# Performance work log

Measured on AMD Instinct MI355X. Metric: run time of the kernel, lower is better.

The kernel has to match this reference:

```python
import jax, jax.numpy as jnp
import numpy as np

B, S, D = 4, 1024, 2048
NH, HD = 16, 128  # nhead, head_dim
SCALE = HD ** -0.5


def setup_inputs() -> dict:
    key = jax.random.key(0)
    ks = jax.random.split(key, 7)
    query = jax.random.normal(ks[0], (B, S, D), dtype=jnp.float32)
    key_t = jax.random.normal(ks[1], (B, S, D), dtype=jnp.float32)
    value = jax.random.normal(ks[2], (B, S, D), dtype=jnp.float32)
    # qkv_proj: Linear(D, 3D) with bias; out_proj: Linear(D, D) with bias
    Wqkv = jax.random.normal(ks[3], (3 * D, D), dtype=jnp.float32) * (D ** -0.5)
    bqkv = jnp.zeros((3 * D,), dtype=jnp.float32)
    Wout = jax.random.normal(ks[4], (D, D), dtype=jnp.float32) * (D ** -0.5)
    bout = jnp.zeros((D,), dtype=jnp.float32)
    return {"query": query, "key": key_t, "value": value,
            "Wqkv": Wqkv, "bqkv": bqkv, "Wout": Wout, "bout": bout}


def reference(query, key, value, Wqkv, bqkv, Wout, bout):
    # NOTE: module ignores `key`/`value` args; qkv comes from query alone.
    b, s, d = query.shape
    qkv = query @ Wqkv.T + bqkv                       # (B,S,3D)
    q, k, v = jnp.split(qkv, 3, axis=-1)
    q = q.reshape(b, s, NH, HD).transpose(0, 2, 1, 3) * SCALE  # (B,H,S,hd)
    k = k.reshape(b, s, NH, HD).transpose(0, 2, 1, 3)          # (B,H,S,hd)
    # faithful replication of the module's odd v permutation:
    v = v.reshape(b, s, HD, NH).transpose(0, 2, 1, 3)          # (B,hd,S,H)
    v = v.reshape(b, s, NH * HD).reshape(b, s, NH, HD).transpose(0, 2, 1, 3)  # (B,H,S,hd)
    scores = jnp.einsum('bhqd,bhkd->bhqk', q, k)               # (B,H,S,S)
    causal = jnp.triu(jnp.ones((s, s), dtype=bool), k=1)
    scores = jnp.where(causal, -jnp.inf, scores)
    attn = jax.nn.softmax(scores.astype(jnp.float32), axis=-1).astype(query.dtype)
    out = jnp.einsum('bhqk,bhkd->bhqd', attn, v)               # (B,H,S,hd)
    out = out.transpose(0, 2, 1, 3).reshape(b, s, d)
    return out @ Wout.T + bout
```

## Files before the change

kernel.cpp:

```cpp
#include <hip/hip_runtime.h>
#include <hip/hip_bf16.h>
#include <stdint.h>

typedef __bf16 bf16x8 __attribute__((ext_vector_type(8)));
typedef float  floatx4 __attribute__((ext_vector_type(4)));

#define NEG_BIG (-1e30f)

#define GLD16(g, l) __builtin_amdgcn_global_load_lds(                         \
    (__attribute__((address_space(1))) void*)(g),                             \
    (__attribute__((address_space(3))) void*)(l), 16, 0, 0)

__device__ __forceinline__ void cvt16(const float* __restrict__ s,
                                      __hip_bfloat16* __restrict__ d) {
    float4 f[4];
#pragma unroll
    for (int i = 0; i < 4; i++) f[i] = ((const float4*)s)[i];
    union { __hip_bfloat16 h[16]; uint4 u[2]; } o;
#pragma unroll
    for (int i = 0; i < 4; i++) {
        o.h[4 * i + 0] = __float2bfloat16(f[i].x);
        o.h[4 * i + 1] = __float2bfloat16(f[i].y);
        o.h[4 * i + 2] = __float2bfloat16(f[i].z);
        o.h[4 * i + 3] = __float2bfloat16(f[i].w);
    }
    ((uint4*)d)[0] = o.u[0];
    ((uint4*)d)[1] = o.u[1];
}

__global__ __launch_bounds__(256)
void cvt3_f32_bf16(const float* __restrict__ a, size_t na8,
                   const float* __restrict__ b, size_t nb8,
                   const float* __restrict__ c, size_t nc8,
                   __hip_bfloat16* __restrict__ da,
                   __hip_bfloat16* __restrict__ db,
                   __hip_bfloat16* __restrict__ dc)
{
    const size_t total  = na8 + nb8 + nc8;
    const size_t stride = (size_t)gridDim.x * blockDim.x;
    for (size_t idx = (size_t)blockIdx.x * blockDim.x + threadIdx.x;
         idx < total; idx += stride) {
        const float* s; __hip_bfloat16* d; size_t o;
        if (idx < na8)            { s = a; d = da; o = idx; }
        else if (idx < na8 + nb8) { s = b; d = db; o = idx - na8; }
        else                      { s = c; d = dc; o = idx - na8 - nb8; }
        const float4 f0 = ((const float4*)s)[o * 2 + 0];
        const float4 f1 = ((const float4*)s)[o * 2 + 1];
        union { __hip_bfloat16 h[8]; uint4 u; } z;
        z.h[0] = __float2bfloat16(f0.x); z.h[1] = __float2bfloat16(f0.y);
        z.h[2] = __float2bfloat16(f0.z); z.h[3] = __float2bfloat16(f0.w);
        z.h[4] = __float2bfloat16(f1.x); z.h[5] = __float2bfloat16(f1.y);
        z.h[6] = __float2bfloat16(f1.z); z.h[7] = __float2bfloat16(f1.w);
        ((uint4*)d)[o] = z.u;
    }
}

template <bool OUT_F32>
__global__ __launch_bounds__(512, 2)
void gemm8p_nt_bias(const __hip_bfloat16* __restrict__ A,
                    const __hip_bfloat16* __restrict__ B,
                    const float* __restrict__ bias, void* __restrict__ Cv,
                    int M, int N, int K, int lda, int ldb, int nby)
{
    __shared__ __align__(16) __hip_bfloat16 Asm[2][128 * 64];
    __shared__ __align__(16) __hip_bfloat16 Bsm[2][256 * 64];

    const int nwg = gridDim.x, cpx = nwg >> 3;
    const int flat = blockIdx.x;
    const int swz  = (flat & 7) * cpx + (flat >> 3);
    const int by = swz % nby, bx = swz / nby;
    const int m0 = by * 128, n0 = bx * 256;

    const int t    = threadIdx.x;
    const int wave = t >> 6, lane = t & 63;
    const int quad = lane >> 4, l16 = lane & 15;
    const int wr   = wave >> 2, wc = wave & 3;
    const int NT   = K >> 6;

    const int l8 = lane >> 3;
    const int g_ = (lane & 7) ^ l8;
    const int aRowBase = (wave >> 2) * 64 + (wave & 3) * 8;
    const int bRowBase = wave * 8;

    auto stageA = [&](int tk, int j, int buf) {
        GLD16(A + (size_t)(m0 + aRowBase + j * 32 + l8) * lda + tk * 64 + g_ * 8,
              &Asm[buf][0] + (aRowBase + j * 32) * 64);
    };
    auto stageB = [&](int tk, int j, int buf) {
        GLD16(B + (size_t)(n0 + bRowBase + j * 64 + l8) * ldb + tk * 64 + g_ * 8,
              &Bsm[buf][0] + (bRowBase + j * 64) * 64);
    };

    const int g0 = (quad ^ (l16 & 7)) << 3;

    floatx4 acc[4][4];
    const floatx4 zero = {0.f, 0.f, 0.f, 0.f};
#pragma unroll
    for (int mi = 0; mi < 4; mi++)
#pragma unroll
        for (int ni = 0; ni < 4; ni++) acc[mi][ni] = zero;

    stageA(0, 0, 0); stageA(0, 1, 0);
    stageB(0, 0, 0); stageB(0, 1, 0); stageB(0, 2, 0); stageB(0, 3, 0);
    if (NT > 1) {
        stageA(1, 0, 1); stageB(1, 0, 1); stageB(1, 1, 1);
        asm volatile("s_waitcnt vmcnt(3)" ::: "memory");
    } else {
        asm volatile("s_waitcnt vmcnt(0)" ::: "memory");
    }
    __syncthreads();

    int cb = 0;
    for (int tk = 0; tk < NT; ++tk, cb ^= 1) {
        const __hip_bfloat16* Ab = &Asm[cb][0];
        const __hip_bfloat16* Bb = &Bsm[cb][0];
        const int nb = cb ^ 1;

        bf16x8 af[2][2], bfr[4][2];
#pragma unroll
        for (int i = 0; i < 2; i++)
#pragma unroll
            for (int ks = 0; ks < 2; ks++)
                af[i][ks] = *(const bf16x8*)(
                    Ab + (wr * 64 + i * 16 + l16) * 64 + (g0 ^ (ks ? 32 : 0)));
#pragma unroll
        for (int ni = 0; ni < 4; ni++)
#pragma unroll
            for (int ks = 0; ks < 2; ks++)
                bfr[ni][ks] = *(const bf16x8*)(
                    Bb + (wc * 64 + ni * 16 + l16) * 64 + (g0 ^ (ks ? 32 : 0)));
        if (tk + 1 < NT) {
            stageA(tk + 1, 1, nb); stageB(tk + 1, 2, nb); stageB(tk + 1, 3, nb);
        }
        __builtin_amdgcn_s_barrier();
        asm volatile("s_waitcnt lgkmcnt(0)" ::: "memory");
        __builtin_amdgcn_s_setprio(1);
#pragma unroll
        for (int ks = 0; ks < 2; ks++)
#pragma unroll
            for (int i = 0; i < 2; i++)
#pragma unroll
                for (int ni = 0; ni < 4; ni++)
                    acc[i][ni] = __builtin_amdgcn_mfma_f32_16x16x32_bf16(
                        af[i][ks], bfr[ni][ks], acc[i][ni], 0, 0, 0);
        __builtin_amdgcn_s_setprio(0);
        __builtin_amdgcn_s_barrier();

#pragma unroll
        for (int i = 0; i < 2; i++)
#pragma unroll
            for (int ks = 0; ks < 2; ks++)
                af[i][ks] = *(const bf16x8*)(
                    Ab + (wr * 64 + (2 + i) * 16 + l16) * 64 + (g0 ^ (ks ? 32 : 0)));
        if (tk + 2 < NT) {
            stageA(tk + 2, 0, cb); stageB(tk + 2, 0, cb); stageB(tk + 2, 1, cb);
        }
        __builtin_amdgcn_s_barrier();
        asm volatile("s_waitcnt lgkmcnt(0)" ::: "memory");
        __builtin_amdgcn_s_setprio(1);
#pragma unroll
        for (int ks = 0; ks < 2; ks++)
#pragma unroll
            for (int i = 0; i < 2; i++)
#pragma unroll
                for (int ni = 0; ni < 4; ni++)
                    acc[2 + i][ni] = __builtin_amdgcn_mfma_f32_16x16x32_bf16(
                        af[i][ks], bfr[ni][ks], acc[2 + i][ni], 0, 0, 0);
        __builtin_amdgcn_s_setprio(0);
        if (tk + 2 < NT)
            asm volatile("s_waitcnt vmcnt(3)" ::: "memory");
        else if (tk + 1 < NT)
            asm volatile("s_waitcnt vmcnt(0)" ::: "memory");
        __builtin_amdgcn_s_barrier();
    }

#pragma unroll
    for (int mi = 0; mi < 4; mi++) {
        const int row = m0 + wr * 64 + mi * 16 + quad * 4;
#pragma unroll
        for (int ni = 0; ni < 4; ni++) {
            const int col = n0 + wc * 64 + ni * 16 + l16;
            const float bv = bias[col];
#pragma unroll
            for (int r = 0; r < 4; r++) {
                const float v = acc[mi][ni][r] + bv;
                if (OUT_F32)
                    ((float*)Cv)[(size_t)(row + r) * N + col] = v;
                else
                    ((__hip_bfloat16*)Cv)[(size_t)(row + r) * N + col] =
                        __float2bfloat16(v);
            }
        }
    }
}

template <bool A_F32, bool B_F32, bool OUT_F32>
__global__ __launch_bounds__(256, 2)
void gemm_nt_bias(const void* __restrict__ Av, const void* __restrict__ Bv,
                  const float* __restrict__ bias, void* __restrict__ Cv,
                  int M, int N, int K, int lda, int ldb)
{
    __shared__ __align__(16) __hip_bfloat16 Asm[128 * 32];
    __shared__ __align__(16) __hip_bfloat16 Bsm[128 * 32];
    const int m0   = blockIdx.y * 128;
    const int n0   = blockIdx.x * 128;
    const int t    = threadIdx.x;
    const int wave = t >> 6, lane = t & 63;
    const int quad = lane >> 4, l16 = lane & 15;
    const int wr   = wave >> 1, wc = wave & 1;

    floatx4 zero = {0.f, 0.f, 0.f, 0.f};
    floatx4 acc[4][4];
    for (int i = 0; i < 4; i++)
        for (int j = 0; j < 4; j++) acc[i][j] = zero;

    for (int k0 = 0; k0 < K; k0 += 32) {
        if (A_F32) {
            const float* A = (const float*)Av;
            const int row = t >> 1, half = t & 1;
            cvt16(A + (size_t)(m0 + row) * lda + k0 + half * 16,
                  Asm + row * 32 + half * 16);
        } else {
            const __hip_bfloat16* A = (const __hip_bfloat16*)Av;
            for (int j = 0; j < 2; ++j) {
                const int chunk = (wave * 2 + j) * 64 + lane;
                const int row   = chunk >> 2;
                const int kc    = chunk & 3;
                GLD16(A + (size_t)(m0 + row) * lda + k0 + kc * 8,
                      Asm + (wave * 2 + j) * 512);
            }
        }
        if (B_F32) {
            const float* B = (const float*)Bv;
            const int row = t >> 1, half = t & 1;
            cvt16(B + (size_t)(n0 + row) * ldb + k0 + half * 16,
                  Bsm + row * 32 + half * 16);
        } else {
            const __hip_bfloat16* B = (const __hip_bfloat16*)Bv;
            for (int j = 0; j < 2; ++j) {
                const int chunk = (wave * 2 + j) * 64 + lane;
                const int row   = chunk >> 2;
                const int kc    = chunk & 3;
                GLD16(B + (size_t)(n0 + row) * ldb + k0 + kc * 8,
                      Bsm + (wave * 2 + j) * 512);
            }
        }
        __syncthreads();

        bf16x8 af[4], bf[4];
        for (int i = 0; i < 4; i++) {
            af[i] = *(const bf16x8*)(Asm + (wr * 64 + i * 16 + l16) * 32 + quad * 8);
            bf[i] = *(const bf16x8*)(Bsm + (wc * 64 + i * 16 + l16) * 32 + quad * 8);
        }
        for (int mi = 0; mi < 4; mi++)
            for (int ni = 0; ni < 4; ni++)
                acc[mi][ni] = __builtin_amdgcn_mfma_f32_16x16x32_bf16(
                    af[mi], bf[ni], acc[mi][ni], 0, 0, 0);
        __syncthreads();
    }

    for (int mi = 0; mi < 4; mi++) {
        const int row = m0 + wr * 64 + mi * 16 + quad * 4;
        for (int ni = 0; ni < 4; ni++) {
            const int col = n0 + wc * 64 + ni * 16 + l16;
            const float bv = bias[col];
            for (int r = 0; r < 4; r++) {
                const float v = acc[mi][ni][r] + bv;
                if (OUT_F32)
                    ((float*)Cv)[(size_t)(row + r) * N + col] = v;
                else
                    ((__hip_bfloat16*)Cv)[(size_t)(row + r) * N + col] =
                        __float2bfloat16(v);
            }
        }
    }
}

__global__ __launch_bounds__(256)
void permute_v(const __hip_bfloat16* __restrict__ QKV,
               __hip_bfloat16* __restrict__ Vpt)
{
    __shared__ __align__(16) __hip_bfloat16 S[64 * 64];
    const int blk = blockIdx.x;
    const int sb = blk & 31, h = (blk >> 5) & 15, b = blk >> 9;
    const int t = threadIdx.x;

    for (int j = 0; j < 2; j++) {
        const int chunk = j * 256 + t;
        const int lrow  = chunk >> 3;
        const int lcol  = (chunk & 7) * 8;
        const int r8 = lrow >> 3, jj = lrow & 7;
        const int srow = r8 * 128 + h * 8 + jj;
        const int scol = sb * 64 + lcol;
        *(uint4*)(S + chunk * 8) =
            *(const uint4*)(QKV + ((size_t)(b * 1024) + srow) * 6144 + 4096 + scol);
    }
    __syncthreads();

    const size_t obase = (((size_t)(b * 16 + h)) * 32 + sb) * 4096;
    for (int i = 0; i < 16; i++) {
        const int lin = t + 256 * i;
        const int hd = lin >> 5, ss = lin & 31;
        Vpt[obase + lin] =
            S[((ss & 7) * 8 + (hd >> 4)) * 64 + (ss >> 3) * 16 + (hd & 15)];
    }
}

__global__ __launch_bounds__(256, 2)
void flash_attn(const __hip_bfloat16* __restrict__ QKV,
                const __hip_bfloat16* __restrict__ Vpt,
                __hip_bfloat16* __restrict__ O)
{
    __shared__ __align__(16) __hip_bfloat16 Kt[2][64 * 128];
    __shared__ __align__(16) __hip_bfloat16 Vt[2][2 * 128 * 32];
    __shared__ __align__(16) __hip_bfloat16 Pl[64 * 64];

    const int bid  = blockIdx.x;
    const int pair = bid >> 6;
    const int g    = bid & 63;
    const int b    = g >> 4, h = g & 15;
    const int t    = threadIdx.x;
    const int wave = t >> 6, lane = t & 63;
    const int quad = lane >> 4, l16 = lane & 15;
    const float scale = 0.08838834764831845f;

    const int    rowb  = b * 1024;
    const size_t vbase = (((size_t)(b * 16 + h)) * 32) * 4096;
    const floatx4 zero = {0.f, 0.f, 0.f, 0.f};

    auto stageK = [&](int tk, int bufi) {
        const int kv0 = tk * 64;
        __hip_bfloat16* dst = &Kt[bufi][0];
#pragma unroll
        for (int j = 0; j < 4; j++) {
            const int c0 = (wave * 4 + j) * 64 + lane;
            const int r  = c0 >> 4;
            const int gg = (c0 & 15) ^ (r & 7);
            GLD16(QKV + ((size_t)(rowb + kv0 + r)) * 6144 + 2048 + h * 128 + gg * 8,
                  dst + (wave * 4 + j) * 512);
        }
    };
    auto stageV = [&](int tk, int bufi) {
        const __hip_bfloat16* src = Vpt + vbase + (size_t)(tk * 2) * 4096;
        __hip_bfloat16* dst = &Vt[bufi][0];
#pragma unroll
        for (int j = 0; j < 4; j++) {
            const int c0   = (wave * 4 + j) * 64 + lane;
            const int half = c0 >> 9, w = c0 & 511;
            const int r    = w >> 2;
            const int gg   = (w & 3) ^ (r & 3);
            GLD16(src + half * 4096 + r * 32 + gg * 8,
                  dst + (wave * 4 + j) * 512);
        }
    };

    for (int ph = 0; ph < 2; ++ph) {
        const int qb = ph ? (15 - pair) * 64 : pair * 64;
        const int nt = ph ? 16 - pair       : pair + 1;

        bf16x8 qf[4];
        {
            const size_t rb = ((size_t)(rowb + qb + wave * 16 + l16)) * 6144 + h * 128;
#pragma unroll
            for (int kc = 0; kc < 4; kc++)
                qf[kc] = *(const bf16x8*)(QKV + rb + kc * 32 + quad * 8);
        }

        float m_i[4], l_i[4];
        floatx4 oacc[8];
#pragma unroll
        for (int r = 0; r < 4; r++) { m_i[r] = NEG_BIG; l_i[r] = 0.f; }
#pragma unroll
        for (int ni = 0; ni < 8; ni++) oacc[ni] = zero;

        stageK(0, 0); stageV(0, 0);

        for (int tk = 0; tk < nt; ++tk) {
            const int cur = tk & 1;
            if (tk + 1 < nt) {
                stageK(tk + 1, cur ^ 1); stageV(tk + 1, cur ^ 1);
                asm volatile("s_waitcnt vmcnt(8)" ::: "memory");
            } else {
                asm volatile("s_waitcnt vmcnt(0)" ::: "memory");
            }
            __builtin_amdgcn_s_barrier();
            asm volatile("" ::: "memory");

            const __hip_bfloat16* Kb = &Kt[cur][0];
            const __hip_bfloat16* Vb = &Vt[cur][0];
            const int kv0 = tk * 64;

            floatx4 sc[4];
#pragma unroll
            for (int cbk = 0; cbk < 4; cbk++) {
                floatx4 s = zero;
                const int r  = cbk * 16 + l16;
                const int sw = r & 7;
#pragma unroll
                for (int kc = 0; kc < 4; kc++) {
                    bf16x8 kf = *(const bf16x8*)(
                        Kb + r * 128 + (((kc * 4 + quad) ^ sw) << 3));
                    s = __builtin_amdgcn_mfma_f32_16x16x32_bf16(qf[kc], kf, s, 0, 0, 0);
                }
                sc[cbk] = s;
            }

            const int qrow = qb + wave * 16 + quad * 4;
            if (tk == nt - 1) {
#pragma unroll
                for (int rr = 0; rr < 4; rr++)
#pragma unroll
                    for (int cbk = 0; cbk < 4; cbk++) {
                        const int col = kv0 + cbk * 16 + l16;
                        const float v = sc[cbk][rr] * scale;
                        sc[cbk][rr] = (col > qrow + rr) ? NEG_BIG : v;
                    }
            } else {
#pragma unroll
                for (int rr = 0; rr < 4; rr++)
#pragma unroll
                    for (int cbk = 0; cbk < 4; cbk++) sc[cbk][rr] *= scale;
            }
            float mx[4];
#pragma unroll
            for (int rr = 0; rr < 4; rr++)
                mx[rr] = fmaxf(fmaxf(sc[0][rr], sc[1][rr]),
                               fmaxf(sc[2][rr], sc[3][rr]));
#pragma unroll
            for (int off = 1; off < 16; off <<= 1)
#pragma unroll
                for (int rr = 0; rr < 4; rr++)
                    mx[rr] = fmaxf(mx[rr], __shfl_xor(mx[rr], off));

            float alpha[4], rsum[4];
#pragma unroll
            for (int rr = 0; rr < 4; rr++) {
                const float mnew = fmaxf(m_i[rr], mx[rr]);
                alpha[rr] = __expf(m_i[rr] - mnew);
                m_i[rr] = mnew;
                float acc = 0.f;
#pragma unroll
                for (int cbk = 0; cbk < 4; cbk++) {
                    const float pv = __expf(sc[cbk][rr] - mnew);
                    sc[cbk][rr] = pv;
                    acc += pv;
                }
                rsum[rr] = acc;
            }
#pragma unroll
            for (int off = 1; off < 16; off <<= 1)
#pragma unroll
                for (int rr = 0; rr < 4; rr++)
                    rsum[rr] += __shfl_xor(rsum[rr], off);
#pragma unroll
            for (int rr = 0; rr < 4; rr++)
                l_i[rr] = l_i[rr] * alpha[rr] + rsum[rr];
#pragma unroll
            for (int ni = 0; ni < 8; ni++)
#pragma unroll
                for (int rr = 0; rr < 4; rr++) oacc[ni][rr] *= alpha[rr];

#pragma unroll
            for (int cbk = 0; cbk < 4; cbk++)
#pragma unroll
                for (int rr = 0; rr < 4; rr++) {
                    const int row = wave * 16 + quad * 4 + rr;
                    const int col = cbk * 16 + l16;
                    Pl[row * 64 + ((((col >> 3) ^ (row & 7)) << 3) | (col & 7))] =
                        __float2bfloat16(sc[cbk][rr]);
                }
            asm volatile("s_waitcnt lgkmcnt(0)" ::: "memory");

            const int prow = wave * 16 + l16;
            bf16x8 pf[2];
#pragma unroll
            for (int kc = 0; kc < 2; kc++)
                pf[kc] = *(const bf16x8*)(
                    Pl + prow * 64 + (((kc * 4 + quad) ^ (prow & 7)) << 3));
#pragma unroll
            for (int ni = 0; ni < 8; ni++) {
                const int vr = ni * 16 + l16;
#pragma unroll
                for (int kc = 0; kc < 2; kc++) {
                    bf16x8 vf = *(const bf16x8*)(
                        Vb + kc * 4096 + vr * 32 + (((quad ^ (vr & 3))) << 3));
                    oacc[ni] = __builtin_amdgcn_mfma_f32_16x16x32_bf16(
                        pf[kc], vf, oacc[ni], 0, 0, 0);
                }
            }

            asm volatile("" ::: "memory");
            __builtin_amdgcn_s_barrier();
            asm volatile("" ::: "memory");
        }

        float inv[4];
#pragma unroll
        for (int rr = 0; rr < 4; rr++) inv[rr] = 1.0f / l_i[rr];
#pragma unroll
        for (int ni = 0; ni < 8; ni++)
#pragma unroll
            for (int rr = 0; rr < 4; rr++) {
                const int row = qb + wave * 16 + quad * 4 + rr;
                O[((size_t)rowb + row) * 6144 + 4096 + h * 128 + ni * 16 + l16] =
                    __float2bfloat16(oacc[ni][rr] * inv[rr]);
            }
    }
}

extern "C" void kernel_launch(void* const* d_in, const int* in_sizes, int n_in,
                              void* d_out, int out_size, void* d_ws, size_t ws_size,
                              hipStream_t stream) {
    const float* query = (const float*)d_in[0];
    const float* Wqkv = (const float*)d_in[3];
    const float* bqkv = (const float*)d_in[4];
    const float* Wout = (const float*)d_in[5];
    const float* bout = (const float*)d_in[6];
    float* out = (float*)d_out;

    const size_t MB = 1048576;
    char* ws = (char*)d_ws;
    __hip_bfloat16* QKV = (__hip_bfloat16*)ws;
    __hip_bfloat16* Vpt = (__hip_bfloat16*)(ws + 48 * MB);
    __hip_bfloat16* Att = QKV + 4096;

    dim3 blk(256);

    if (ws_size >= 113 * MB) {
        __hip_bfloat16* Qbf     = (__hip_bfloat16*)(ws + 64 * MB);
        __hip_bfloat16* Wqkv_bf = (__hip_bfloat16*)(ws + 80 * MB);
        __hip_bfloat16* Wout_bf = (__hip_bfloat16*)(ws + 104 * MB);

        cvt3_f32_bf16<<<dim3(2048), blk, 0, stream>>>(
            query, (size_t)4096 * 2048 / 8,
            Wqkv,  (size_t)6144 * 2048 / 8,
            Wout,  (size_t)2048 * 2048 / 8,
            Qbf, Wqkv_bf, Wout_bf);
        gemm8p_nt_bias<false><<<dim3(768), dim3(512), 0, stream>>>(
            Qbf, Wqkv_bf, bqkv, QKV, 4096, 6144, 2048, 2048, 2048, 32);
        permute_v<<<dim3(2048), blk, 0, stream>>>(QKV, Vpt);
        flash_attn<<<dim3(512), blk, 0, stream>>>(QKV, Vpt, QKV);
        gemm8p_nt_bias<true><<<dim3(256), dim3(512), 0, stream>>>(
            Att, Wout_bf, bout, out, 4096, 2048, 2048, 6144, 2048, 32);
    } else {
        gemm_nt_bias<true, true, false><<<dim3(48, 32), blk, 0, stream>>>(
            query, Wqkv, bqkv, QKV, 4096, 6144, 2048, 2048, 2048);
        permute_v<<<dim3(2048), blk, 0, stream>>>(QKV, Vpt);
        flash_attn<<<dim3(512), blk, 0, stream>>>(QKV, Vpt, QKV);
        gemm_nt_bias<false, true, true><<<dim3(16, 32), blk, 0, stream>>>(
            Att, Wout, bout, out, 4096, 2048, 2048, 6144, 2048);
    }
}
```

Baseline: 381.1 us.

## Add 128x192-tile 256-thread GEMM for QKV projection with split-phase pipelining

Introduces a new bf16 NT GEMM kernel using 128x192 output tiles, 4 waves of 256 threads, and a two-phase per-k-tile schedule that interleaves global-to-LDS staging of the next tiles with MFMA work on half the A rows. The QKV projection launch switches from the 512-thread 128x256 kernel (768 blocks) to this kernel with 1024 blocks and an explicit XCD-aware block mapping. The aim is a better tile count against CU count (fewer tail waves) and overlap of loads with compute. The cost is more B-fragment registers per wave and a hand-tuned vmcnt/barrier sequence that must match the issued load counts exactly.

```diff
diff --git a/kernel.cpp b/kernel.cpp
--- a/kernel.cpp
+++ b/kernel.cpp
@@ -55,6 +55,143 @@
     }
 }
 
+__global__ __launch_bounds__(256, 2)
+void gemm2b_nt_bias(const __hip_bfloat16* __restrict__ A,
+                    const __hip_bfloat16* __restrict__ B,
+                    const float* __restrict__ bias,
+                    __hip_bfloat16* __restrict__ C,
+                    int M, int N, int K, int lda, int ldb)
+{
+    __shared__ __align__(16) __hip_bfloat16 Asm[2][128 * 64];
+    __shared__ __align__(16) __hip_bfloat16 Bsm[2][192 * 64];
+
+    const int flat = blockIdx.x;
+    const int c    = flat & 7;
+    const int i_   = flat >> 3;
+    const int by = (c & 1) * 16 + (i_ & 15);
+    const int bx = (c >> 1) * 8 + (i_ >> 4);
+    const int m0 = by * 128, n0 = bx * 192;
+
+    const int t    = threadIdx.x;
+    const int wave = t >> 6, lane = t & 63;
+    const int quad = lane >> 4, l16 = lane & 15;
+    const int wr   = wave >> 1, wc = wave & 1;
+    const int NT   = K >> 6;
+
+    const int l8 = lane >> 3;
+    const int g_ = (lane & 7) ^ l8;
+    auto stageA = [&](int tk, int j, int buf) {
+        GLD16(A + (size_t)(m0 + j * 32 + wave * 8 + l8) * lda + tk * 64 + g_ * 8,
+              &Asm[buf][0] + (j * 32 + wave * 8) * 64);
+    };
+    auto stageB = [&](int tk, int j, int buf) {
+        GLD16(B + (size_t)(n0 + j * 32 + wave * 8 + l8) * ldb + tk * 64 + g_ * 8,
+              &Bsm[buf][0] + (j * 32 + wave * 8) * 64);
+    };
+
+    const int g0 = (quad ^ (l16 & 7)) << 3;
+
+    floatx4 acc[4][6];
+    const floatx4 zero = {0.f, 0.f, 0.f, 0.f};
+#pragma unroll
+    for (int mi = 0; mi < 4; mi++)
+#pragma unroll
+        for (int ni = 0; ni < 6; ni++) acc[mi][ni] = zero;
+
+#pragma unroll
+    for (int j = 0; j < 4; j++) stageA(0, j, 0);
+#pragma unroll
+    for (int j = 0; j < 6; j++) stageB(0, j, 0);
+    if (NT > 1) {
+        stageA(1, 0, 1); stageA(1, 2, 1);
+        stageB(1, 0, 1); stageB(1, 1, 1); stageB(1, 2, 1);
+        asm volatile("s_waitcnt vmcnt(5)" ::: "memory");
+    } else {
+        asm volatile("s_waitcnt vmcnt(0)" ::: "memory");
+    }
+    __syncthreads();
+
+    int cb = 0;
+    for (int tk = 0; tk < NT; ++tk, cb ^= 1) {
+        const __hip_bfloat16* Ab = &Asm[cb][0];
+        const __hip_bfloat16* Bb = &Bsm[cb][0];
+        const int nb = cb ^ 1;
+
+        bf16x8 af[2][2], bfr[6][2];
+#pragma unroll
+        for (int i = 0; i < 2; i++)
+#pragma unroll
+            for (int ks = 0; ks < 2; ks++)
+                af[i][ks] = *(const bf16x8*)(
+                    Ab + (wr * 64 + i * 16 + l16) * 64 + (g0 ^ (ks ? 32 : 0)));
+#pragma unroll
+        for (int ni = 0; ni < 6; ni++)
+#pragma unroll
+            for (int ks = 0; ks < 2; ks++)
+                bfr[ni][ks] = *(const bf16x8*)(
+                    Bb + (wc * 96 + ni * 16 + l16) * 64 + (g0 ^ (ks ? 32 : 0)));
+        if (tk + 1 < NT) {
+            stageA(tk + 1, 1, nb); stageA(tk + 1, 3, nb);
+            stageB(tk + 1, 3, nb); stageB(tk + 1, 4, nb); stageB(tk + 1, 5, nb);
+        }
+        __builtin_amdgcn_s_barrier();
+        asm volatile("s_waitcnt lgkmcnt(0)" ::: "memory");
+        __builtin_amdgcn_s_setprio(1);
+#pragma unroll
+        for (int ks = 0; ks < 2; ks++)
+#pragma unroll
+            for (int i = 0; i < 2; i++)
+#pragma unroll
+                for (int ni = 0; ni < 6; ni++)
+                    acc[i][ni] = __builtin_amdgcn_mfma_f32_16x16x32_bf16(
+                        af[i][ks], bfr[ni][ks], acc[i][ni], 0, 0, 0);
+        __builtin_amdgcn_s_setprio(0);
+        __builtin_amdgcn_s_barrier();
+
+#pragma unroll
+        for (int i = 0; i < 2; i++)
+#pragma unroll
+            for (int ks = 0; ks < 2; ks++)
+                af[i][ks] = *(const bf16x8*)(
+                    Ab + (wr * 64 + (2 + i) * 16 + l16) * 64 + (g0 ^ (ks ? 32 : 0)));
+        if (tk + 2 < NT) {
+            stageA(tk + 2, 0, cb); stageA(tk + 2, 2, cb);
+            stageB(tk + 2, 0, cb); stageB(tk + 2, 1, cb); stageB(tk + 2, 2, cb);
+        }
+        __builtin_amdgcn_s_barrier();
+        asm volatile("s_waitcnt lgkmcnt(0)" ::: "memory");
+        __builtin_amdgcn_s_setprio(1);
+#pragma unroll
+        for (int ks = 0; ks < 2; ks++)
+#pragma unroll
+            for (int i = 0; i < 2; i++)
+#pragma unroll
+                for (int ni = 0; ni < 6; ni++)
+                    acc[2 + i][ni] = __builtin_amdgcn_mfma_f32_16x16x32_bf16(
+                        af[i][ks], bfr[ni][ks], acc[2 + i][ni], 0, 0, 0);
+        __builtin_amdgcn_s_setprio(0);
+        if (tk + 2 < NT)
+            asm volatile("s_waitcnt vmcnt(5)" ::: "memory");
+        else if (tk + 1 < NT)
+            asm volatile("s_waitcnt vmcnt(0)" ::: "memory");
+        __builtin_amdgcn_s_barrier();
+    }
+
+#pragma unroll
+    for (int mi = 0; mi < 4; mi++) {
+        const int row = m0 + wr * 64 + mi * 16 + quad * 4;
+#pragma unroll
+        for (int ni = 0; ni < 6; ni++) {
+            const int col = n0 + wc * 96 + ni * 16 + l16;
+            const float bv = bias[col];
+#pragma unroll
+            for (int r = 0; r < 4; r++)
+                C[(size_t)(row + r) * N + col] =
+                    __float2bfloat16(acc[mi][ni][r] + bv);
+        }
+    }
+}
+
 template <bool OUT_F32>
 __global__ __launch_bounds__(512, 2)
 void gemm8p_nt_bias(const __hip_bfloat16* __restrict__ A,
@@ -536,8 +673,8 @@
             Wqkv,  (size_t)6144 * 2048 / 8,
             Wout,  (size_t)2048 * 2048 / 8,
             Qbf, Wqkv_bf, Wout_bf);
-        gemm8p_nt_bias<false><<<dim3(768), dim3(512), 0, stream>>>(
-            Qbf, Wqkv_bf, bqkv, QKV, 4096, 6144, 2048, 2048, 2048, 32);
+        gemm2b_nt_bias<<<dim3(1024), dim3(256), 0, stream>>>(
+            Qbf, Wqkv_bf, bqkv, QKV, 4096, 6144, 2048, 2048, 2048);
         permute_v<<<dim3(2048), blk, 0, stream>>>(QKV, Vpt);
         flash_attn<<<dim3(512), blk, 0, stream>>>(QKV, Vpt, QKV);
         gemm8p_nt_bias<true><<<dim3(256), dim3(512), 0, stream>>>(
```

New measurement: 358.1 us. 1.06x faster.
